# Optimization experiments

Measured on AMD Instinct MI355X. Metric: run time of the kernel, lower is better.

The kernel has to match this reference:

```python
import jax, jax.numpy as jnp
import numpy as np

LEAK = 0.2  # LeakyReLU alpha

def setup_inputs() -> dict:
    key = jax.random.key(0)
    k1, k2, k3, k4 = jax.random.split(key, 4)
    B, N, D, H = 4, 1024, 64, 64
    qs = jax.random.normal(k1, (B, N, D), dtype=jnp.float32)
    ks = jax.random.normal(k2, (B, N, D), dtype=jnp.float32)
    vs = jax.random.normal(k3, (B, N, D), dtype=jnp.float32)
    W = jax.random.normal(k4, (3 * D, H), dtype=jnp.float32) * 0.05  # Dense kernel on concat(q,k,q-k)
    b = jnp.zeros((H,), dtype=jnp.float32)
    a = jnp.ones((H,), dtype=jnp.float32)
    return {"qs": qs, "ks": ks, "vs": vs, "W": W, "b": b, "a": a}

def reference(qs, ks, vs, W, b, a):
    D = qs.shape[-1]
    norm = 1.0 / jnp.sqrt(jnp.asarray(D, dtype=qs.dtype))
    # Dense on concat(q, k, q-k) splits as q@(Wq+Wd) + k@(Wk-Wd) + b,
    # avoiding the O(N^2 * 3D) concat tensor (same math as TF concat->Dense).
    Wq, Wk, Wd = W[:D], W[D:2 * D], W[2 * D:]
    hq = qs @ (Wq + Wd)            # [B, N, H]  query-side term
    hk = ks @ (Wk - Wd)            # [B, N, H]  key-side term
    h = hq[:, :, None, :] + hk[:, None, :, :] + b   # [B, N, N, H]
    h = jnp.where(h > 0, h, LEAK * h)               # LeakyReLU(0.2)
    scores = jnp.einsum('bijh,h->bij', h, a) * norm # [B, N, N]
    att = jax.nn.softmax(scores, axis=-1)
    return jnp.matmul(att, vs)                      # [B, N, D]
```

## Files before the change

kernel.cpp:

```cpp
#include <hip/hip_runtime.h>
#include <math.h>

#define LOG2E 1.4426950408889634f
typedef __attribute__((ext_vector_type(2))) _Float16 h2v;

static __device__ __forceinline__ unsigned pkrtz_u32(float lo, float hi) {
  auto p = __builtin_amdgcn_cvt_pkrtz(lo, hi);
  unsigned u; __builtin_memcpy(&u, &p, 4); return u;
}
static __device__ __forceinline__ h2v habs2(h2v x) {
  unsigned u; __builtin_memcpy(&u, &x, 4);
  u &= 0x7FFF7FFFu;
  h2v r; __builtin_memcpy(&r, &u, 4); return r;
}
static __device__ __forceinline__ h2v u2h(unsigned u) {
  h2v r; __builtin_memcpy(&r, &u, 4); return r;
}


__global__ __launch_bounds__(256) void prep_kernel(
    const float* __restrict__ qs, const float* __restrict__ ks,
    const float* __restrict__ W, const float* __restrict__ bias,
    const float* __restrict__ a,
    unsigned* __restrict__ hq2, uint4* __restrict__ khT4,
    float* __restrict__ Dj, unsigned* __restrict__ abd2) {
  __shared__ __align__(16) float wcomb[64][68];
  __shared__ __align__(16) float xin[64][68];
  const int blk = blockIdx.x;
  const bool qpart = blk < 64;
  const int r0 = (qpart ? blk : blk - 64) * 64;
  const int t = threadIdx.x;
  const float* src = qpart ? qs : ks;
  if (blk == 0 && t < 32) {
    abd2[t] = pkrtz_u32(0.05f * a[2 * t], 0.05f * a[2 * t + 1]);
  }
  for (int rep = 0; rep < 16; ++rep) {
    int e = rep * 256 + t;
    int row = e >> 6, col = e & 63;
    float wd = W[(128 + row) * 64 + col];
    float wm = qpart ? (W[row * 64 + col] + wd)
                     : (W[(64 + row) * 64 + col] - wd);
    wcomb[row][col] = wm;
    xin[row][col] = src[(r0 + row) * 64 + col];
  }
  __syncthreads();
  const int r = t >> 2;
  const int h0 = (t & 3) << 4;
  float acc[16];
#pragma unroll
  for (int k = 0; k < 16; ++k) acc[k] = 0.f;
#pragma unroll 8
  for (int d = 0; d < 64; ++d) {
    float xv = xin[r][d];
#pragma unroll
    for (int c = 0; c < 4; ++c) {
      float4 w4 = *(const float4*)&wcomb[d][h0 + (c << 2)];
      acc[c * 4 + 0] = fmaf(xv, w4.x, acc[c * 4 + 0]);
      acc[c * 4 + 1] = fmaf(xv, w4.y, acc[c * 4 + 1]);
      acc[c * 4 + 2] = fmaf(xv, w4.z, acc[c * 4 + 2]);
      acc[c * 4 + 3] = fmaf(xv, w4.w, acc[c * 4 + 3]);
    }
  }
  int grow = r0 + r;
  if (qpart) {
    unsigned pr[8];
#pragma unroll
    for (int i = 0; i < 8; ++i) pr[i] = pkrtz_u32(acc[2 * i], acc[2 * i + 1]);
    uint4* dst = (uint4*)&hq2[grow * 32 + (t & 3) * 8];
    dst[0] = make_uint4(pr[0], pr[1], pr[2], pr[3]);
    dst[1] = make_uint4(pr[4], pr[5], pr[6], pr[7]);
  } else {
    int bidx = grow >> 10;
    int j = grow & 1023;
    float val[16];
    float part = 0.f;
#pragma unroll
    for (int k = 0; k < 16; ++k) {
      val[k] = acc[k] + bias[h0 + k];
      part += a[h0 + k] * val[k];
    }
    part += __shfl_xor(part, 1);
    part += __shfl_xor(part, 2);
    if ((t & 3) == 0) Dj[bidx * 1024 + j] = 0.075f * part;
    unsigned pr[8];
#pragma unroll
    for (int i = 0; i < 8; ++i) pr[i] = pkrtz_u32(val[2 * i], val[2 * i + 1]);
    const int h4a = (t & 3) * 2;
    khT4[(bidx * 8 + h4a) * 1024 + j]     = make_uint4(pr[0], pr[1], pr[2], pr[3]);
    khT4[(bidx * 8 + h4a + 1) * 1024 + j] = make_uint4(pr[4], pr[5], pr[6], pr[7]);
  }
}

__global__ __launch_bounds__(256) void attn10_kernel(
    const float* __restrict__ vs,
    const unsigned* __restrict__ hq2, const uint4* __restrict__ khT4,
    const float* __restrict__ Dj, const unsigned* __restrict__ abd2,
    float* __restrict__ out) {
  __shared__ __align__(16) float plds[4][1024];
  __shared__ __align__(16) unsigned q2lds[4 * 32];
  __shared__ __align__(16) unsigned ab2lds[32];
  __shared__ float redm[4][4];
  __shared__ float redl[4][4];

  const int t = threadIdx.x;
  const int lane = t & 63;
  const int w = t >> 6;
  const int b = blockIdx.y;
  const int rowbase = blockIdx.x * 4;
  const int growbase = b * 1024 + rowbase;

  const uint4* kh_b = khT4 + (size_t)b * 8 * 1024;
  const float* v_b = vs + b * 1024 * 64;

  if (t < 128) q2lds[t] = hq2[growbase * 32 + t];
  if (t >= 128 && t < 160) ab2lds[t - 128] = abd2[t - 128];
  __syncthreads();

  const int jloc = w * 256 + lane * 4;
  float4 d4 = *(const float4*)(Dj + b * 1024 + jloc);

  float s[4][4];
#pragma unroll
  for (int r = 0; r < 4; ++r)
#pragma unroll
    for (int c = 0; c < 4; ++c) s[r][c] = 0.f;

  uint4 kc0 = kh_b[jloc], kc1 = kh_b[jloc + 1], kc2 = kh_b[jloc + 2],
        kc3 = kh_b[jloc + 3];
#pragma unroll 1
  for (int it = 0; it < 8; ++it) {
    const int nx = (it < 7) ? it + 1 : it;
    uint4 kn0 = kh_b[nx * 1024 + jloc];
    uint4 kn1 = kh_b[nx * 1024 + jloc + 1];
    uint4 kn2 = kh_b[nx * 1024 + jloc + 2];
    uint4 kn3 = kh_b[nx * 1024 + jloc + 3];
    uint4 abq = *(const uint4*)&ab2lds[it * 4];
    const unsigned abu[4] = {abq.x, abq.y, abq.z, abq.w};
    const unsigned kcu[4][4] = {{kc0.x, kc0.y, kc0.z, kc0.w},
                                {kc1.x, kc1.y, kc1.z, kc1.w},
                                {kc2.x, kc2.y, kc2.z, kc2.w},
                                {kc3.x, kc3.y, kc3.z, kc3.w}};
#pragma unroll
    for (int r = 0; r < 4; ++r) {
      uint4 qq = *(const uint4*)&q2lds[r * 32 + it * 4];
      const unsigned qu[4] = {qq.x, qq.y, qq.z, qq.w};
#pragma unroll
      for (int u = 0; u < 4; ++u) {
        h2v qh = u2h(qu[u]);
        h2v a2 = u2h(abu[u]);
#pragma unroll
        for (int c = 0; c < 4; ++c) {
          h2v x = habs2(qh + u2h(kcu[c][u]));
          s[r][c] = __builtin_amdgcn_fdot2(a2, x, s[r][c], false);
        }
      }
    }
    kc0 = kn0; kc1 = kn1; kc2 = kn2; kc3 = kn3;
  }
#pragma unroll
  for (int r = 0; r < 4; ++r) {
    s[r][0] += d4.x; s[r][1] += d4.y; s[r][2] += d4.z; s[r][3] += d4.w;
  }

#pragma unroll
  for (int r = 0; r < 4; ++r) {
    float m = fmaxf(fmaxf(s[r][0], s[r][1]), fmaxf(s[r][2], s[r][3]));
#pragma unroll
    for (int off = 32; off >= 1; off >>= 1) m = fmaxf(m, __shfl_xor(m, off));
    if (lane == 0) redm[r][w] = m;
  }
  __syncthreads();
  float mx[4];
#pragma unroll
  for (int r = 0; r < 4; ++r) {
    float4 rm = *(const float4*)&redm[r][0];
    mx[r] = fmaxf(fmaxf(rm.x, rm.y), fmaxf(rm.z, rm.w));
  }
#pragma unroll
  for (int r = 0; r < 4; ++r) {
    float p0 = __builtin_amdgcn_exp2f((s[r][0] - mx[r]) * LOG2E);
    float p1 = __builtin_amdgcn_exp2f((s[r][1] - mx[r]) * LOG2E);
    float p2 = __builtin_amdgcn_exp2f((s[r][2] - mx[r]) * LOG2E);
    float p3 = __builtin_amdgcn_exp2f((s[r][3] - mx[r]) * LOG2E);
    float4 pw; pw.x = p0; pw.y = p1; pw.z = p2; pw.w = p3;
    *(float4*)&plds[r][jloc] = pw;
    float ps = (p0 + p1) + (p2 + p3);
#pragma unroll
    for (int off = 32; off >= 1; off >>= 1) ps += __shfl_xor(ps, off);
    if (lane == 0) redl[r][w] = ps;
  }
  __syncthreads();

  const int jsub = lane >> 4;
  const int dq = (lane & 15) * 4;
  const int cbase = w * 256;
  float o[4][4];
#pragma unroll
  for (int r = 0; r < 4; ++r)
#pragma unroll
    for (int dd = 0; dd < 4; ++dd) o[r][dd] = 0.f;

#pragma unroll 2
  for (int step = 0; step < 16; ++step) {
    int j = cbase + step * 16 + jsub * 4;
    float4 v0 = *(const float4*)(v_b + (j + 0) * 64 + dq);
    float4 v1 = *(const float4*)(v_b + (j + 1) * 64 + dq);
    float4 v2 = *(const float4*)(v_b + (j + 2) * 64 + dq);
    float4 v3 = *(const float4*)(v_b + (j + 3) * 64 + dq);
#pragma unroll
    for (int r = 0; r < 4; ++r) {
      float4 p4 = *(const float4*)&plds[r][j];
      o[r][0] = fmaf(p4.x, v0.x, o[r][0]); o[r][1] = fmaf(p4.x, v0.y, o[r][1]);
      o[r][2] = fmaf(p4.x, v0.z, o[r][2]); o[r][3] = fmaf(p4.x, v0.w, o[r][3]);
      o[r][0] = fmaf(p4.y, v1.x, o[r][0]); o[r][1] = fmaf(p4.y, v1.y, o[r][1]);
      o[r][2] = fmaf(p4.y, v1.z, o[r][2]); o[r][3] = fmaf(p4.y, v1.w, o[r][3]);
      o[r][0] = fmaf(p4.z, v2.x, o[r][0]); o[r][1] = fmaf(p4.z, v2.y, o[r][1]);
      o[r][2] = fmaf(p4.z, v2.z, o[r][2]); o[r][3] = fmaf(p4.z, v2.w, o[r][3]);
      o[r][0] = fmaf(p4.w, v3.x, o[r][0]); o[r][1] = fmaf(p4.w, v3.y, o[r][1]);
      o[r][2] = fmaf(p4.w, v3.z, o[r][2]); o[r][3] = fmaf(p4.w, v3.w, o[r][3]);
    }
  }
  __syncthreads();

#pragma unroll
  for (int r = 0; r < 4; ++r)
#pragma unroll
    for (int dd = 0; dd < 4; ++dd) {
      o[r][dd] += __shfl_xor(o[r][dd], 16);
      o[r][dd] += __shfl_xor(o[r][dd], 32);
    }
  float* ob = &plds[0][0];
  if (lane < 16) {
#pragma unroll
    for (int r = 0; r < 4; ++r) {
      float4 ov; ov.x = o[r][0]; ov.y = o[r][1]; ov.z = o[r][2]; ov.w = o[r][3];
      *(float4*)&ob[(w * 4 + r) * 64 + dq] = ov;
    }
  }
  __syncthreads();
  {
    int r = t >> 6, d = t & 63;
    float ax = 0.f;
#pragma unroll
    for (int wv = 0; wv < 4; ++wv) ax += ob[(wv * 4 + r) * 64 + d];
    float4 rl = *(const float4*)&redl[r][0];
    float inv = 1.f / ((rl.x + rl.y) + (rl.z + rl.w));
    out[(growbase + r) * 64 + d] = ax * inv;
  }
}

extern "C" void kernel_launch(void* const* d_in, const int* in_sizes, int n_in,
                              void* d_out, int out_size, void* d_ws, size_t ws_size,
                              hipStream_t stream) {
  const float* qs = (const float*)d_in[0];
  const float* ks = (const float*)d_in[1];
  const float* vs = (const float*)d_in[2];
  const float* W  = (const float*)d_in[3];
  const float* bi = (const float*)d_in[4];
  const float* a  = (const float*)d_in[5];
  float* out = (float*)d_out;
  unsigned* hq2   = (unsigned*)d_ws;
  uint4*    khT4  = (uint4*)((char*)d_ws + 524288);
  float*    Dj    = (float*)((char*)d_ws + 1048576);
  unsigned* abd2  = (unsigned*)((char*)d_ws + 1064960);
  prep_kernel<<<128, 256, 0, stream>>>(qs, ks, W, bi, a, hq2, khT4, Dj, abd2);
  attn10_kernel<<<dim3(256, 4), 256, 0, stream>>>(vs, hq2, khT4, Dj, abd2, out);
}
```

Baseline: 37.31 us.

## Compute P·V with fp16 MFMA using pre-packed V fragments

Replaces the scalar FMA P·V loop with MFMA 16x16x32 f16 instructions. Probabilities are stored to LDS as packed half precision. A new vpack kernel converts V to fp16 in the MFMA B-fragment layout ahead of time, which removes the cross-lane shuffle reduction and halves P's LDS footprint. The cost is an extra kernel launch, added workspace traffic, and fp16 rounding of P and V. Only lanes 0-15 write results, which relies on the row-group mapping of the MFMA output.

```diff
diff --git a/kernel.cpp b/kernel.cpp
--- a/kernel.cpp
+++ b/kernel.cpp
@@ -3,6 +3,8 @@
 
 #define LOG2E 1.4426950408889634f
 typedef __attribute__((ext_vector_type(2))) _Float16 h2v;
+typedef __attribute__((ext_vector_type(8))) _Float16 f16x8;
+typedef __attribute__((ext_vector_type(4))) float f32x4;
 
 static __device__ __forceinline__ unsigned pkrtz_u32(float lo, float hi) {
   auto p = __builtin_amdgcn_cvt_pkrtz(lo, hi);
@@ -91,12 +93,30 @@
   }
 }
 
-__global__ __launch_bounds__(256) void attn10_kernel(
-    const float* __restrict__ vs,
+__global__ __launch_bounds__(256) void vpack_kernel(
+    const float* __restrict__ vs, uint4* __restrict__ vfrag) {
+  const int unit = blockIdx.x;
+  const int b = unit >> 5, kstep = unit & 31;
+  const int t = threadIdx.x;
+  const int lane = t & 63, ntile = t >> 6;
+  const int j0 = kstep * 32 + (lane >> 4) * 8;
+  const int d = ntile * 16 + (lane & 15);
+  const float* vb = vs + b * 1024 * 64;
+  unsigned pr[4];
+#pragma unroll
+  for (int i = 0; i < 4; ++i)
+    pr[i] = pkrtz_u32(vb[(j0 + 2 * i) * 64 + d], vb[(j0 + 2 * i + 1) * 64 + d]);
+  vfrag[((b * 32 + kstep) * 4 + ntile) * 64 + lane] =
+      make_uint4(pr[0], pr[1], pr[2], pr[3]);
+}
+
+__global__ __launch_bounds__(256) void attn11_kernel(
+    const uint4* __restrict__ vfrag,
     const unsigned* __restrict__ hq2, const uint4* __restrict__ khT4,
     const float* __restrict__ Dj, const unsigned* __restrict__ abd2,
     float* __restrict__ out) {
-  __shared__ __align__(16) float plds[4][1024];
+  __shared__ __align__(16) unsigned p2u[4 * 520];
+  __shared__ __align__(16) float ob[16 * 64];
   __shared__ __align__(16) unsigned q2lds[4 * 32];
   __shared__ __align__(16) unsigned ab2lds[32];
   __shared__ float redm[4][4];
@@ -110,7 +130,7 @@
   const int growbase = b * 1024 + rowbase;
 
   const uint4* kh_b = khT4 + (size_t)b * 8 * 1024;
-  const float* v_b = vs + b * 1024 * 64;
+  const uint4* vf_b = vfrag + (size_t)b * 32 * 4 * 64;
 
   if (t < 128) q2lds[t] = hq2[growbase * 32 + t];
   if (t >= 128 && t < 160) ab2lds[t - 128] = abd2[t - 128];
@@ -182,8 +202,8 @@
     float p1 = __builtin_amdgcn_exp2f((s[r][1] - mx[r]) * LOG2E);
     float p2 = __builtin_amdgcn_exp2f((s[r][2] - mx[r]) * LOG2E);
     float p3 = __builtin_amdgcn_exp2f((s[r][3] - mx[r]) * LOG2E);
-    float4 pw; pw.x = p0; pw.y = p1; pw.z = p2; pw.w = p3;
-    *(float4*)&plds[r][jloc] = pw;
+    *(uint2*)&p2u[r * 520 + (jloc >> 1)] =
+        make_uint2(pkrtz_u32(p0, p1), pkrtz_u32(p2, p3));
     float ps = (p0 + p1) + (p2 + p3);
 #pragma unroll
     for (int off = 32; off >= 1; off >>= 1) ps += __shfl_xor(ps, off);
@@ -191,51 +211,31 @@
   }
   __syncthreads();
 
-  const int jsub = lane >> 4;
-  const int dq = (lane & 15) * 4;
-  const int cbase = w * 256;
-  float o[4][4];
-#pragma unroll
-  for (int r = 0; r < 4; ++r)
-#pragma unroll
-    for (int dd = 0; dd < 4; ++dd) o[r][dd] = 0.f;
-
+  f32x4 acc[4];
+#pragma unroll
+  for (int nt = 0; nt < 4; ++nt) acc[nt] = (f32x4){0.f, 0.f, 0.f, 0.f};
+  const int arow = (lane & 3) * 520;
+  const int kgr = (lane >> 4) * 8;
 #pragma unroll 2
-  for (int step = 0; step < 16; ++step) {
-    int j = cbase + step * 16 + jsub * 4;
-    float4 v0 = *(const float4*)(v_b + (j + 0) * 64 + dq);
-    float4 v1 = *(const float4*)(v_b + (j + 1) * 64 + dq);
-    float4 v2 = *(const float4*)(v_b + (j + 2) * 64 + dq);
-    float4 v3 = *(const float4*)(v_b + (j + 3) * 64 + dq);
-#pragma unroll
-    for (int r = 0; r < 4; ++r) {
-      float4 p4 = *(const float4*)&plds[r][j];
-      o[r][0] = fmaf(p4.x, v0.x, o[r][0]); o[r][1] = fmaf(p4.x, v0.y, o[r][1]);
-      o[r][2] = fmaf(p4.x, v0.z, o[r][2]); o[r][3] = fmaf(p4.x, v0.w, o[r][3]);
-      o[r][0] = fmaf(p4.y, v1.x, o[r][0]); o[r][1] = fmaf(p4.y, v1.y, o[r][1]);
-      o[r][2] = fmaf(p4.y, v1.z, o[r][2]); o[r][3] = fmaf(p4.y, v1.w, o[r][3]);
-      o[r][0] = fmaf(p4.z, v2.x, o[r][0]); o[r][1] = fmaf(p4.z, v2.y, o[r][1]);
-      o[r][2] = fmaf(p4.z, v2.z, o[r][2]); o[r][3] = fmaf(p4.z, v2.w, o[r][3]);
-      o[r][0] = fmaf(p4.w, v3.x, o[r][0]); o[r][1] = fmaf(p4.w, v3.y, o[r][1]);
-      o[r][2] = fmaf(p4.w, v3.z, o[r][2]); o[r][3] = fmaf(p4.w, v3.w, o[r][3]);
-    }
-  }
-  __syncthreads();
-
-#pragma unroll
-  for (int r = 0; r < 4; ++r)
-#pragma unroll
-    for (int dd = 0; dd < 4; ++dd) {
-      o[r][dd] += __shfl_xor(o[r][dd], 16);
-      o[r][dd] += __shfl_xor(o[r][dd], 32);
-    }
-  float* ob = &plds[0][0];
+  for (int ks = 0; ks < 8; ++ks) {
+    const int j0 = w * 256 + ks * 32;
+    uint4 au = *(const uint4*)&p2u[arow + ((j0 + kgr) >> 1)];
+    f16x8 af; __builtin_memcpy(&af, &au, 16);
+    const int gks = j0 >> 5;
+#pragma unroll
+    for (int nt = 0; nt < 4; ++nt) {
+      uint4 bu = vf_b[(gks * 4 + nt) * 64 + lane];
+      f16x8 bf; __builtin_memcpy(&bf, &bu, 16);
+      acc[nt] = __builtin_amdgcn_mfma_f32_16x16x32_f16(af, bf, acc[nt], 0, 0, 0);
+    }
+  }
+
   if (lane < 16) {
 #pragma unroll
-    for (int r = 0; r < 4; ++r) {
-      float4 ov; ov.x = o[r][0]; ov.y = o[r][1]; ov.z = o[r][2]; ov.w = o[r][3];
-      *(float4*)&ob[(w * 4 + r) * 64 + dq] = ov;
-    }
+    for (int nt = 0; nt < 4; ++nt)
+#pragma unroll
+      for (int rg = 0; rg < 4; ++rg)
+        ob[(w * 4 + rg) * 64 + nt * 16 + lane] = acc[nt][rg];
   }
   __syncthreads();
   {
@@ -263,6 +263,8 @@
   uint4*    khT4  = (uint4*)((char*)d_ws + 524288);
   float*    Dj    = (float*)((char*)d_ws + 1048576);
   unsigned* abd2  = (unsigned*)((char*)d_ws + 1064960);
+  uint4*    vfrag = (uint4*)((char*)d_ws + 1065216);
   prep_kernel<<<128, 256, 0, stream>>>(qs, ks, W, bi, a, hq2, khT4, Dj, abd2);
-  attn10_kernel<<<dim3(256, 4), 256, 0, stream>>>(vs, hq2, khT4, Dj, abd2, out);
-}
+  vpack_kernel<<<128, 256, 0, stream>>>(vs, vfrag);
+  attn11_kernel<<<dim3(256, 4), 256, 0, stream>>>(vfrag, hq2, khT4, Dj, abd2, out);
+}
```

New measurement: 38.14 us. +2.2%, slower.
